# Kernel optimization log

Hardware: AMD Instinct MI355X
Metric: run time of the kernel (lower is better)

The kernel has to match this reference:

```python
import jax, jax.numpy as jnp
import numpy as np

NUM_HEADS = 16
LN_EPS = 1e-5


def setup_inputs() -> dict:
    key = jax.random.key(0)
    ks = jax.random.split(key, 6)
    b, s, d = 2, 2048, 1024
    scale = 1.0 / np.sqrt(d)
    return {
        "x": jax.random.normal(ks[0], (b, s, d), dtype=jnp.float32),
        "W_w": jax.random.normal(ks[1], (3 * d, d), dtype=jnp.float32) * scale,
        "W_b": jax.random.normal(ks[2], (3 * d,), dtype=jnp.float32) * 0.01,
        "proj_w": jax.random.normal(ks[3], (d, d), dtype=jnp.float32) * scale,
        "proj_b": jax.random.normal(ks[4], (d,), dtype=jnp.float32) * 0.01,
        "gamma": jnp.ones((d,), dtype=jnp.float32),
        "beta": jnp.zeros((d,), dtype=jnp.float32),
    }


def reference(x, W_w, W_b, proj_w, proj_b, gamma, beta):
    b, s, d = x.shape
    h = NUM_HEADS
    hd = d // h
    # fused QKV projection: [b,s,3d]
    qkv = x @ W_w.T + W_b
    q, k, v = jnp.split(qkv, 3, axis=-1)
    # [b,s,d] -> [b,h,s,hd]
    q, k, v = (z.reshape(b, s, h, hd).transpose(0, 2, 1, 3) for z in (q, k, v))
    # NOTE: original scales by sqrt(d), not sqrt(head_dim)
    attn = jnp.einsum('bhqd,bhkd->bhqk', q, k) / jnp.sqrt(jnp.asarray(d, x.dtype))
    attn_weights = jax.nn.softmax(attn, axis=-1)  # [b,h,s,s]
    o = jnp.einsum('bhqk,bhkd->bhqd', attn_weights, v)
    o = o.transpose(0, 2, 1, 3).reshape(b, s, d)
    out = o @ proj_w.T + proj_b  # dropout is identity at eval
    y = x + out
    mu = jnp.mean(y, axis=-1, keepdims=True)
    var = jnp.var(y, axis=-1, keepdims=True)
    y_norm = (y - mu) / jnp.sqrt(var + LN_EPS) * gamma + beta
    return (y_norm, attn_weights)
```

## Files before the change

### kernel.cpp

```cpp
#include <hip/hip_runtime.h>
#include <cstdint>

#define BB 2
#define SS 2048
#define DD 1024
#define HH 16
#define HDIM 64
#define MM (BB*SS)
#define N3 (3*DD)

typedef __attribute__((ext_vector_type(4))) float f32x4;
typedef __attribute__((ext_vector_type(8))) __bf16 bf16x8;

static __device__ __forceinline__ unsigned short f2bf_fast(float f) {
  __bf16 h = (__bf16)f;
  return __builtin_bit_cast(unsigned short, h);
}

static __device__ __forceinline__ uint4 pack8f(const float4 a, const float4 b) {
  union { unsigned short us[8]; uint4 v; } pk;
  pk.us[0] = f2bf_fast(a.x); pk.us[1] = f2bf_fast(a.y); pk.us[2] = f2bf_fast(a.z); pk.us[3] = f2bf_fast(a.w);
  pk.us[4] = f2bf_fast(b.x); pk.us[5] = f2bf_fast(b.y); pk.us[6] = f2bf_fast(b.z); pk.us[7] = f2bf_fast(b.w);
  return pk.v;
}

static __device__ __forceinline__ void gload16(const unsigned short* g, unsigned short* l) {
  __builtin_amdgcn_global_load_lds(
      (const __attribute__((address_space(1))) void*)g,
      (__attribute__((address_space(3))) void*)l, 16, 0, 0);
}

__global__ __launch_bounds__(256) void cvt_kernel(
    const float* __restrict__ x, const float* __restrict__ Ww,
    const float* __restrict__ pw,
    unsigned short* __restrict__ xb, unsigned short* __restrict__ Wwb,
    unsigned short* __restrict__ pwb) {
  const size_t i = ((size_t)blockIdx.x * 256 + threadIdx.x) * 8;
  const float* src;
  unsigned short* dst;
  if (i < 4194304u)       { src = x  + i;            dst = xb  + i; }
  else if (i < 7340032u)  { src = Ww + (i - 4194304u); dst = Wwb + (i - 4194304u); }
  else                    { src = pw + (i - 7340032u); dst = pwb + (i - 7340032u); }
  const float4* s4 = (const float4*)src;
  *(uint4*)dst = pack8f(s4[0], s4[1]);
}

__global__ __launch_bounds__(256) void gemm_qkv(
    const unsigned short* __restrict__ xb, const unsigned short* __restrict__ Wwb,
    const float* __restrict__ Wb,
    unsigned short* __restrict__ qb, unsigned short* __restrict__ kb,
    unsigned short* __restrict__ vbT) {
  __shared__ __align__(16) unsigned short As[128 * 32];
  __shared__ __align__(16) unsigned short Bs[128 * 32];
  const int t = threadIdx.x;
  const int l = t & 63, w = t >> 6;
  const int wr = w >> 1, wc = w & 1;
  const int m0 = blockIdx.y * 128, n0 = blockIdx.x * 128;
  f32x4 acc[4][4] = {};

  for (int kt = 0; kt < DD; kt += 32) {
    __syncthreads();
    #pragma unroll
    for (int i = 0; i < 2; ++i) {
      const int row = (i * 4 + w) * 16 + (l >> 2);
      const int cc = (l & 3) * 8;
      gload16(xb  + (size_t)(m0 + row) * DD + kt + cc, &As[(i * 4 + w) * 512]);
      gload16(Wwb + (size_t)(n0 + row) * DD + kt + cc, &Bs[(i * 4 + w) * 512]);
    }
    __syncthreads();
    bf16x8 a[4], b[4];
    #pragma unroll
    for (int i = 0; i < 4; ++i) {
      a[i] = __builtin_bit_cast(bf16x8, *(const uint4*)&As[(wr * 64 + i * 16 + (l & 15)) * 32 + (l >> 4) * 8]);
      b[i] = __builtin_bit_cast(bf16x8, *(const uint4*)&Bs[(wc * 64 + i * 16 + (l & 15)) * 32 + (l >> 4) * 8]);
    }
    #pragma unroll
    for (int i = 0; i < 4; ++i)
      #pragma unroll
      for (int j = 0; j < 4; ++j)
        acc[i][j] = __builtin_amdgcn_mfma_f32_16x16x32_bf16(a[i], b[j], acc[i][j], 0, 0, 0);
  }

  #pragma unroll
  for (int i = 0; i < 4; ++i)
    #pragma unroll
    for (int j = 0; j < 4; ++j)
      #pragma unroll
      for (int r = 0; r < 4; ++r) {
        const int row = m0 + wr * 64 + i * 16 + (l >> 4) * 4 + r;
        const int col = n0 + wc * 64 + j * 16 + (l & 15);
        const float v = acc[i][j][r] + Wb[col];
        const int bidx = row >> 11;
        const int srow = row & 2047;
        const int which = col >> 10;
        const int cc = col & 1023;
        const int head = cc >> 6;
        const int hd = cc & 63;
        if (which == 0) {
          qb[((size_t)((bidx * HH + head) * SS + srow)) * HDIM + hd] = f2bf_fast(v * 0.04508422f);
        } else if (which == 1) {
          kb[((size_t)((bidx * HH + head) * SS + srow)) * HDIM + hd] = f2bf_fast(v);
        } else {
          vbT[((size_t)(bidx * HH + head) * HDIM + hd) * SS + srow] = f2bf_fast(v);
        }
      }
}

__global__ __launch_bounds__(256) void attn_kernel(
    const unsigned short* __restrict__ qb,
    const unsigned short* __restrict__ kb,
    const unsigned short* __restrict__ vbT,
    unsigned short* __restrict__ ob,
    float* __restrict__ attn_out) {
  __shared__ __align__(16) unsigned short Ks[2][64 * 72];
  __shared__ __align__(16) unsigned short Vts[2][64 * 72];
  __shared__ __align__(16) unsigned short Ps[4 * 16 * 72];
  const int t = threadIdx.x;
  const int l = t & 63, w = t >> 6;
  const int bid = blockIdx.x;
  const int swz = (bid & 7) * 128 + (bid >> 3);
  const int bh = swz >> 5;
  const int q0 = (swz & 31) * 64;
  const size_t base = (size_t)bh * SS * HDIM;

  bf16x8 qa[2];
  #pragma unroll
  for (int kc = 0; kc < 2; ++kc)
    qa[kc] = __builtin_bit_cast(bf16x8,
        *(const uint4*)(qb + base + (size_t)(q0 + w * 16 + (l & 15)) * HDIM + kc * 32 + (l >> 4) * 8));

  const int srow = t >> 2;
  const int scol = (t & 3) * 16;
  const unsigned short* kg = kb + base + (size_t)srow * HDIM + scol;
  const unsigned short* vg = vbT + ((size_t)bh * HDIM + srow) * SS + scol;

  float lsum = 0.f;

  {
    const uint4* g = (const uint4*)kg;
    uint4 a0 = g[0], a1 = g[1];
    uint4* d = (uint4*)&Ks[0][srow * 72 + scol];
    d[0] = a0; d[1] = a1;
  }
  __syncthreads();
  for (int kt = 0; kt < SS; kt += 64) {
    const int cur = (kt >> 6) & 1;
    const bool more = (kt + 64) < SS;
    uint4 a0, a1;
    if (more) {
      const uint4* g = (const uint4*)(kg + (size_t)(kt + 64) * HDIM);
      a0 = g[0]; a1 = g[1];
    }
    f32x4 sf[4] = {};
    __builtin_amdgcn_s_setprio(1);
    #pragma unroll
    for (int kc = 0; kc < 2; ++kc)
      #pragma unroll
      for (int n = 0; n < 4; ++n) {
        bf16x8 kf = __builtin_bit_cast(bf16x8, *(const uint4*)&Ks[cur][(n * 16 + (l & 15)) * 72 + kc * 32 + (l >> 4) * 8]);
        sf[n] = __builtin_amdgcn_mfma_f32_16x16x32_bf16(kf, qa[kc], sf[n], 0, 0, 0);
      }
    __builtin_amdgcn_s_setprio(0);
    #pragma unroll
    for (int n = 0; n < 4; ++n)
      #pragma unroll
      for (int r = 0; r < 4; ++r)
        lsum += __builtin_amdgcn_exp2f(sf[n][r]);
    if (more) {
      uint4* d = (uint4*)&Ks[cur ^ 1][srow * 72 + scol];
      d[0] = a0; d[1] = a1;
    }
    __syncthreads();
  }

  lsum += __shfl_xor(lsum, 16);
  lsum += __shfl_xor(lsum, 32);
  const float rl = 1.0f / lsum;

  f32x4 of[4] = {};
  unsigned short* Pw = &Ps[w * 16 * 72];
  {
    const uint4* g = (const uint4*)kg;
    uint4 a0 = g[0], a1 = g[1];
    const uint4* gv = (const uint4*)vg;
    uint4 b0 = gv[0], b1 = gv[1];
    uint4* d = (uint4*)&Ks[0][srow * 72 + scol];  d[0] = a0; d[1] = a1;
    uint4* dv = (uint4*)&Vts[0][srow * 72 + scol]; dv[0] = b0; dv[1] = b1;
  }
  __syncthreads();
  float* prow = attn_out + ((size_t)bh * SS + (q0 + w * 16 + (l & 15))) * SS + (l >> 4) * 4;
  for (int kt = 0; kt < SS; kt += 64) {
    const int cur = (kt >> 6) & 1;
    const bool more = (kt + 64) < SS;
    uint4 a0, a1, b0, b1;
    if (more) {
      const uint4* g = (const uint4*)(kg + (size_t)(kt + 64) * HDIM);
      a0 = g[0]; a1 = g[1];
      const uint4* gv = (const uint4*)(vg + (kt + 64));
      b0 = gv[0]; b1 = gv[1];
    }
    f32x4 sf[4] = {};
    __builtin_amdgcn_s_setprio(1);
    #pragma unroll
    for (int kc = 0; kc < 2; ++kc)
      #pragma unroll
      for (int n = 0; n < 4; ++n) {
        bf16x8 kf = __builtin_bit_cast(bf16x8, *(const uint4*)&Ks[cur][(n * 16 + (l & 15)) * 72 + kc * 32 + (l >> 4) * 8]);
        sf[n] = __builtin_amdgcn_mfma_f32_16x16x32_bf16(kf, qa[kc], sf[n], 0, 0, 0);
      }
    __builtin_amdgcn_s_setprio(0);
    #pragma unroll
    for (int n = 0; n < 4; ++n) {
      float4 pv;
      pv.x = __builtin_amdgcn_exp2f(sf[n][0]) * rl;
      pv.y = __builtin_amdgcn_exp2f(sf[n][1]) * rl;
      pv.z = __builtin_amdgcn_exp2f(sf[n][2]) * rl;
      pv.w = __builtin_amdgcn_exp2f(sf[n][3]) * rl;
      __builtin_nontemporal_store(*(const f32x4*)&pv, (f32x4*)&prow[kt + n * 16]);
      ushort4 pb4;
      pb4.x = f2bf_fast(pv.x); pb4.y = f2bf_fast(pv.y);
      pb4.z = f2bf_fast(pv.z); pb4.w = f2bf_fast(pv.w);
      *(ushort4*)&Pw[(l & 15) * 72 + n * 16 + (l >> 4) * 4] = pb4;
    }
    #pragma unroll
    for (int kc = 0; kc < 2; ++kc) {
      bf16x8 pa = __builtin_bit_cast(bf16x8, *(const uint4*)&Pw[(l & 15) * 72 + kc * 32 + (l >> 4) * 8]);
      __builtin_amdgcn_s_setprio(1);
      #pragma unroll
      for (int n = 0; n < 4; ++n) {
        bf16x8 vf = __builtin_bit_cast(bf16x8, *(const uint4*)&Vts[cur][(n * 16 + (l & 15)) * 72 + kc * 32 + (l >> 4) * 8]);
        of[n] = __builtin_amdgcn_mfma_f32_16x16x32_bf16(pa, vf, of[n], 0, 0, 0);
      }
      __builtin_amdgcn_s_setprio(0);
    }
    if (more) {
      uint4* d = (uint4*)&Ks[cur ^ 1][srow * 72 + scol];  d[0] = a0; d[1] = a1;
      uint4* dv = (uint4*)&Vts[cur ^ 1][srow * 72 + scol]; dv[0] = b0; dv[1] = b1;
    }
    __syncthreads();
  }

  const int bidx = bh >> 4, h_ = bh & 15;
  #pragma unroll
  for (int n = 0; n < 4; ++n)
    #pragma unroll
    for (int r = 0; r < 4; ++r) {
      const int lr = (l >> 4) * 4 + r;
      const int srw = q0 + w * 16 + lr;
      const int col = h_ * 64 + n * 16 + (l & 15);
      ob[((size_t)bidx * SS + srw) * DD + col] = f2bf_fast(of[n][r]);
    }
}

__global__ __launch_bounds__(256) void gemm_proj(
    const unsigned short* __restrict__ ob, const unsigned short* __restrict__ pwb,
    const float* __restrict__ pb, const float* __restrict__ x,
    float* __restrict__ y) {
  __shared__ __align__(16) unsigned short As[128 * 32];
  __shared__ __align__(16) unsigned short Bs[128 * 32];
  const int t = threadIdx.x;
  const int l = t & 63, w = t >> 6;
  const int wr = w >> 1, wc = w & 1;
  const int m0 = blockIdx.y * 128, n0 = blockIdx.x * 128;
  f32x4 acc[4][4] = {};

  for (int kt = 0; kt < DD; kt += 32) {
    __syncthreads();
    #pragma unroll
    for (int i = 0; i < 2; ++i) {
      const int row = (i * 4 + w) * 16 + (l >> 2);
      const int cc = (l & 3) * 8;
      gload16(ob  + (size_t)(m0 + row) * DD + kt + cc, &As[(i * 4 + w) * 512]);
      gload16(pwb + (size_t)(n0 + row) * DD + kt + cc, &Bs[(i * 4 + w) * 512]);
    }
    __syncthreads();
    bf16x8 a[4], b[4];
    #pragma unroll
    for (int i = 0; i < 4; ++i) {
      a[i] = __builtin_bit_cast(bf16x8, *(const uint4*)&As[(wr * 64 + i * 16 + (l & 15)) * 32 + (l >> 4) * 8]);
      b[i] = __builtin_bit_cast(bf16x8, *(const uint4*)&Bs[(wc * 64 + i * 16 + (l & 15)) * 32 + (l >> 4) * 8]);
    }
    #pragma unroll
    for (int i = 0; i < 4; ++i)
      #pragma unroll
      for (int j = 0; j < 4; ++j)
        acc[i][j] = __builtin_amdgcn_mfma_f32_16x16x32_bf16(a[i], b[j], acc[i][j], 0, 0, 0);
  }
  #pragma unroll
  for (int i = 0; i < 4; ++i)
    #pragma unroll
    for (int j = 0; j < 4; ++j)
      #pragma unroll
      for (int r = 0; r < 4; ++r) {
        const int row = m0 + wr * 64 + i * 16 + (l >> 4) * 4 + r;
        const int col = n0 + wc * 64 + j * 16 + (l & 15);
        const size_t idx = (size_t)row * DD + col;
        y[idx] = acc[i][j][r] + pb[col] + x[idx];
      }
}

__global__ __launch_bounds__(256) void ln_kernel(
    float* __restrict__ y, const float* __restrict__ gamma,
    const float* __restrict__ beta) {
  const int row = blockIdx.x;
  const int t = threadIdx.x;
  const float4 v = ((const float4*)(y + (size_t)row * DD))[t];
  float s  = v.x + v.y + v.z + v.w;
  float s2 = v.x * v.x + v.y * v.y + v.z * v.z + v.w * v.w;
  #pragma unroll
  for (int off = 1; off < 64; off <<= 1) { s += __shfl_xor(s, off); s2 += __shfl_xor(s2, off); }
  __shared__ float red[8];
  const int l = t & 63, w = t >> 6;
  if (l == 0) { red[w] = s; red[4 + w] = s2; }
  __syncthreads();
  s  = red[0] + red[1] + red[2] + red[3];
  s2 = red[4] + red[5] + red[6] + red[7];
  const float mu = s * (1.0f / DD);
  const float var = s2 * (1.0f / DD) - mu * mu;
  const float rs = rsqrtf(var + 1e-5f);
  const float4 g  = ((const float4*)gamma)[t];
  const float4 be = ((const float4*)beta)[t];
  float4 o;
  o.x = (v.x - mu) * rs * g.x + be.x;
  o.y = (v.y - mu) * rs * g.y + be.y;
  o.z = (v.z - mu) * rs * g.z + be.z;
  o.w = (v.w - mu) * rs * g.w + be.w;
  ((float4*)(y + (size_t)row * DD))[t] = o;
}

extern "C" void kernel_launch(void* const* d_in, const int* in_sizes, int n_in,
                              void* d_out, int out_size, void* d_ws, size_t ws_size,
                              hipStream_t stream) {
  const float* x     = (const float*)d_in[0];
  const float* Ww    = (const float*)d_in[1];
  const float* Wb    = (const float*)d_in[2];
  const float* Pw    = (const float*)d_in[3];
  const float* Pb    = (const float*)d_in[4];
  const float* gamma = (const float*)d_in[5];
  const float* beta  = (const float*)d_in[6];

  float* out      = (float*)d_out;
  float* y_norm   = out;
  float* attn_out = out + (size_t)MM * DD;

  char* ws = (char*)d_ws;
  unsigned short* qb  = (unsigned short*)(ws);
  unsigned short* kb  = (unsigned short*)(ws +  8388608);
  unsigned short* vbT = (unsigned short*)(ws + 16777216);
  unsigned short* ob  = (unsigned short*)(ws + 25165824);
  unsigned short* xb  = (unsigned short*)(ws + 33554432);
  unsigned short* Wwb = (unsigned short*)(ws + 41943040);
  unsigned short* pwb = (unsigned short*)(ws + 48234496);

  cvt_kernel<<<4096, 256, 0, stream>>>(x, Ww, Pw, xb, Wwb, pwb);
  gemm_qkv<<<dim3(N3 / 128, MM / 128), 256, 0, stream>>>(xb, Wwb, Wb, qb, kb, vbT);
  attn_kernel<<<1024, 256, 0, stream>>>(qb, kb, vbT, ob, attn_out);
  gemm_proj<<<dim3(DD / 128, MM / 128), 256, 0, stream>>>(ob, pwb, Pb, x, y_norm);
  ln_kernel<<<MM, 256, 0, stream>>>(y_norm, gamma, beta);
}
```

Measured before the change: 266.1 us.

## Split attention key dimension across waves with register-resident K/V tiles

Restructures the attention kernel so that every wave computes all 64 query rows of the block, while each wave handles its own 16-key slice of every 64-key tile. K and V fragments are loaded straight from global memory into registers and prefetched one tile ahead, so the LDS staging buffers and the per-tile barriers go away. Row sums and output partials are combined across waves through LDS at the end. In exchange, the P·V MFMAs run half-empty because the K-operand is zero-padded from 16 to 32 values, register pressure goes up with 16 output accumulators, and the probability stores now cover 16-column slices per wave.

```diff
diff --git a/kernel.cpp b/kernel.cpp
--- a/kernel.cpp
+++ b/kernel.cpp
@@ -112,144 +112,163 @@
     const unsigned short* __restrict__ vbT,
     unsigned short* __restrict__ ob,
     float* __restrict__ attn_out) {
-  __shared__ __align__(16) unsigned short Ks[2][64 * 72];
-  __shared__ __align__(16) unsigned short Vts[2][64 * 72];
-  __shared__ __align__(16) unsigned short Ps[4 * 16 * 72];
+  __shared__ float Ored[4][64][68];
+  __shared__ float Lred[4][64];
   const int t = threadIdx.x;
   const int l = t & 63, w = t >> 6;
+  const int q_l = l & 15, hi = l >> 4;
   const int bid = blockIdx.x;
   const int swz = (bid & 7) * 128 + (bid >> 3);
   const int bh = swz >> 5;
   const int q0 = (swz & 31) * 64;
   const size_t base = (size_t)bh * SS * HDIM;
 
-  bf16x8 qa[2];
-  #pragma unroll
-  for (int kc = 0; kc < 2; ++kc)
-    qa[kc] = __builtin_bit_cast(bf16x8,
-        *(const uint4*)(qb + base + (size_t)(q0 + w * 16 + (l & 15)) * HDIM + kc * 32 + (l >> 4) * 8));
-
-  const int srow = t >> 2;
-  const int scol = (t & 3) * 16;
-  const unsigned short* kg = kb + base + (size_t)srow * HDIM + scol;
-  const unsigned short* vg = vbT + ((size_t)bh * HDIM + srow) * SS + scol;
-
-  float lsum = 0.f;
-
+  bf16x8 qa[4][2];
+  #pragma unroll
+  for (int j = 0; j < 4; ++j)
+    #pragma unroll
+    for (int kc = 0; kc < 2; ++kc)
+      qa[j][kc] = __builtin_bit_cast(bf16x8,
+          *(const uint4*)(qb + base + (size_t)(q0 + j * 16 + q_l) * HDIM + kc * 32 + hi * 8));
+
+  const unsigned short* kga = kb + base + (size_t)(w * 16 + q_l) * HDIM + hi * 8;
+  const unsigned short* vga = vbT + ((size_t)bh * HDIM + q_l) * SS + w * 16 + hi * 4;
+
+  float lsum[4] = {0.f, 0.f, 0.f, 0.f};
   {
-    const uint4* g = (const uint4*)kg;
-    uint4 a0 = g[0], a1 = g[1];
-    uint4* d = (uint4*)&Ks[0][srow * 72 + scol];
-    d[0] = a0; d[1] = a1;
+    uint4 k0 = *(const uint4*)(kga);
+    uint4 k1 = *(const uint4*)(kga + 32);
+    for (int kt = 0; kt < SS; kt += 64) {
+      const bool more = (kt + 64) < SS;
+      uint4 n0, n1;
+      if (more) {
+        n0 = *(const uint4*)(kga + (size_t)(kt + 64) * HDIM);
+        n1 = *(const uint4*)(kga + (size_t)(kt + 64) * HDIM + 32);
+      }
+      f32x4 sQ[4] = {};
+      const bf16x8 kf0 = __builtin_bit_cast(bf16x8, k0);
+      const bf16x8 kf1 = __builtin_bit_cast(bf16x8, k1);
+      __builtin_amdgcn_s_setprio(1);
+      #pragma unroll
+      for (int j = 0; j < 4; ++j) {
+        sQ[j] = __builtin_amdgcn_mfma_f32_16x16x32_bf16(kf0, qa[j][0], sQ[j], 0, 0, 0);
+        sQ[j] = __builtin_amdgcn_mfma_f32_16x16x32_bf16(kf1, qa[j][1], sQ[j], 0, 0, 0);
+      }
+      __builtin_amdgcn_s_setprio(0);
+      #pragma unroll
+      for (int j = 0; j < 4; ++j)
+        #pragma unroll
+        for (int r = 0; r < 4; ++r)
+          lsum[j] += __builtin_amdgcn_exp2f(sQ[j][r]);
+      k0 = n0; k1 = n1;
+    }
+  }
+  #pragma unroll
+  for (int j = 0; j < 4; ++j) {
+    float s = lsum[j];
+    s += __shfl_xor(s, 16);
+    s += __shfl_xor(s, 32);
+    lsum[j] = s;
+  }
+  if (hi == 0) {
+    #pragma unroll
+    for (int j = 0; j < 4; ++j) Lred[w][j * 16 + q_l] = lsum[j];
   }
   __syncthreads();
-  for (int kt = 0; kt < SS; kt += 64) {
-    const int cur = (kt >> 6) & 1;
-    const bool more = (kt + 64) < SS;
-    uint4 a0, a1;
-    if (more) {
-      const uint4* g = (const uint4*)(kg + (size_t)(kt + 64) * HDIM);
-      a0 = g[0]; a1 = g[1];
-    }
-    f32x4 sf[4] = {};
-    __builtin_amdgcn_s_setprio(1);
-    #pragma unroll
-    for (int kc = 0; kc < 2; ++kc)
-      #pragma unroll
-      for (int n = 0; n < 4; ++n) {
-        bf16x8 kf = __builtin_bit_cast(bf16x8, *(const uint4*)&Ks[cur][(n * 16 + (l & 15)) * 72 + kc * 32 + (l >> 4) * 8]);
-        sf[n] = __builtin_amdgcn_mfma_f32_16x16x32_bf16(kf, qa[kc], sf[n], 0, 0, 0);
-      }
-    __builtin_amdgcn_s_setprio(0);
-    #pragma unroll
-    for (int n = 0; n < 4; ++n)
-      #pragma unroll
-      for (int r = 0; r < 4; ++r)
-        lsum += __builtin_amdgcn_exp2f(sf[n][r]);
-    if (more) {
-      uint4* d = (uint4*)&Ks[cur ^ 1][srow * 72 + scol];
-      d[0] = a0; d[1] = a1;
-    }
-    __syncthreads();
-  }
-
-  lsum += __shfl_xor(lsum, 16);
-  lsum += __shfl_xor(lsum, 32);
-  const float rl = 1.0f / lsum;
-
-  f32x4 of[4] = {};
-  unsigned short* Pw = &Ps[w * 16 * 72];
+  float rl[4];
+  #pragma unroll
+  for (int j = 0; j < 4; ++j)
+    rl[j] = 1.0f / (Lred[0][j * 16 + q_l] + Lred[1][j * 16 + q_l] +
+                    Lred[2][j * 16 + q_l] + Lred[3][j * 16 + q_l]);
+
+  float* pbs[4];
+  #pragma unroll
+  for (int j = 0; j < 4; ++j)
+    pbs[j] = attn_out + ((size_t)bh * SS + (q0 + j * 16 + q_l)) * SS + w * 16 + hi * 4;
+
+  f32x4 of[4][4] = {};
   {
-    const uint4* g = (const uint4*)kg;
-    uint4 a0 = g[0], a1 = g[1];
-    const uint4* gv = (const uint4*)vg;
-    uint4 b0 = gv[0], b1 = gv[1];
-    uint4* d = (uint4*)&Ks[0][srow * 72 + scol];  d[0] = a0; d[1] = a1;
-    uint4* dv = (uint4*)&Vts[0][srow * 72 + scol]; dv[0] = b0; dv[1] = b1;
-  }
+    uint4 k0 = *(const uint4*)(kga);
+    uint4 k1 = *(const uint4*)(kga + 32);
+    uint2 vv[4];
+    #pragma unroll
+    for (int d4 = 0; d4 < 4; ++d4)
+      vv[d4] = *(const uint2*)(vga + (size_t)(d4 * 16) * SS);
+    for (int kt = 0; kt < SS; kt += 64) {
+      const bool more = (kt + 64) < SS;
+      uint4 n0, n1; uint2 nv[4];
+      if (more) {
+        n0 = *(const uint4*)(kga + (size_t)(kt + 64) * HDIM);
+        n1 = *(const uint4*)(kga + (size_t)(kt + 64) * HDIM + 32);
+        #pragma unroll
+        for (int d4 = 0; d4 < 4; ++d4)
+          nv[d4] = *(const uint2*)(vga + (size_t)(d4 * 16) * SS + kt + 64);
+      }
+      f32x4 sQ[4] = {};
+      const bf16x8 kf0 = __builtin_bit_cast(bf16x8, k0);
+      const bf16x8 kf1 = __builtin_bit_cast(bf16x8, k1);
+      __builtin_amdgcn_s_setprio(1);
+      #pragma unroll
+      for (int j = 0; j < 4; ++j) {
+        sQ[j] = __builtin_amdgcn_mfma_f32_16x16x32_bf16(kf0, qa[j][0], sQ[j], 0, 0, 0);
+        sQ[j] = __builtin_amdgcn_mfma_f32_16x16x32_bf16(kf1, qa[j][1], sQ[j], 0, 0, 0);
+      }
+      __builtin_amdgcn_s_setprio(0);
+      bf16x8 pbp[4];
+      #pragma unroll
+      for (int j = 0; j < 4; ++j) {
+        float4 pv;
+        pv.x = __builtin_amdgcn_exp2f(sQ[j][0]) * rl[j];
+        pv.y = __builtin_amdgcn_exp2f(sQ[j][1]) * rl[j];
+        pv.z = __builtin_amdgcn_exp2f(sQ[j][2]) * rl[j];
+        pv.w = __builtin_amdgcn_exp2f(sQ[j][3]) * rl[j];
+        __builtin_nontemporal_store(*(const f32x4*)&pv, (f32x4*)(pbs[j] + kt));
+        union { unsigned short us[8]; uint4 v; } pk;
+        pk.us[0] = f2bf_fast(pv.x); pk.us[1] = f2bf_fast(pv.y);
+        pk.us[2] = f2bf_fast(pv.z); pk.us[3] = f2bf_fast(pv.w);
+        pk.us[4] = 0; pk.us[5] = 0; pk.us[6] = 0; pk.us[7] = 0;
+        pbp[j] = __builtin_bit_cast(bf16x8, pk.v);
+      }
+      __builtin_amdgcn_s_setprio(1);
+      #pragma unroll
+      for (int d4 = 0; d4 < 4; ++d4) {
+        uint4 vp; vp.x = vv[d4].x; vp.y = vv[d4].y; vp.z = 0u; vp.w = 0u;
+        const bf16x8 vfp = __builtin_bit_cast(bf16x8, vp);
+        #pragma unroll
+        for (int j = 0; j < 4; ++j)
+          of[d4][j] = __builtin_amdgcn_mfma_f32_16x16x32_bf16(vfp, pbp[j], of[d4][j], 0, 0, 0);
+      }
+      __builtin_amdgcn_s_setprio(0);
+      k0 = n0; k1 = n1;
+      #pragma unroll
+      for (int d4 = 0; d4 < 4; ++d4) vv[d4] = nv[d4];
+    }
+  }
+
+  #pragma unroll
+  for (int d4 = 0; d4 < 4; ++d4)
+    #pragma unroll
+    for (int j = 0; j < 4; ++j)
+      *(f32x4*)&Ored[w][j * 16 + q_l][d4 * 16 + hi * 4] = of[d4][j];
   __syncthreads();
-  float* prow = attn_out + ((size_t)bh * SS + (q0 + w * 16 + (l & 15))) * SS + (l >> 4) * 4;
-  for (int kt = 0; kt < SS; kt += 64) {
-    const int cur = (kt >> 6) & 1;
-    const bool more = (kt + 64) < SS;
-    uint4 a0, a1, b0, b1;
-    if (more) {
-      const uint4* g = (const uint4*)(kg + (size_t)(kt + 64) * HDIM);
-      a0 = g[0]; a1 = g[1];
-      const uint4* gv = (const uint4*)(vg + (kt + 64));
-      b0 = gv[0]; b1 = gv[1];
-    }
-    f32x4 sf[4] = {};
-    __builtin_amdgcn_s_setprio(1);
-    #pragma unroll
-    for (int kc = 0; kc < 2; ++kc)
-      #pragma unroll
-      for (int n = 0; n < 4; ++n) {
-        bf16x8 kf = __builtin_bit_cast(bf16x8, *(const uint4*)&Ks[cur][(n * 16 + (l & 15)) * 72 + kc * 32 + (l >> 4) * 8]);
-        sf[n] = __builtin_amdgcn_mfma_f32_16x16x32_bf16(kf, qa[kc], sf[n], 0, 0, 0);
-      }
-    __builtin_amdgcn_s_setprio(0);
-    #pragma unroll
-    for (int n = 0; n < 4; ++n) {
-      float4 pv;
-      pv.x = __builtin_amdgcn_exp2f(sf[n][0]) * rl;
-      pv.y = __builtin_amdgcn_exp2f(sf[n][1]) * rl;
-      pv.z = __builtin_amdgcn_exp2f(sf[n][2]) * rl;
-      pv.w = __builtin_amdgcn_exp2f(sf[n][3]) * rl;
-      __builtin_nontemporal_store(*(const f32x4*)&pv, (f32x4*)&prow[kt + n * 16]);
-      ushort4 pb4;
-      pb4.x = f2bf_fast(pv.x); pb4.y = f2bf_fast(pv.y);
-      pb4.z = f2bf_fast(pv.z); pb4.w = f2bf_fast(pv.w);
-      *(ushort4*)&Pw[(l & 15) * 72 + n * 16 + (l >> 4) * 4] = pb4;
-    }
-    #pragma unroll
-    for (int kc = 0; kc < 2; ++kc) {
-      bf16x8 pa = __builtin_bit_cast(bf16x8, *(const uint4*)&Pw[(l & 15) * 72 + kc * 32 + (l >> 4) * 8]);
-      __builtin_amdgcn_s_setprio(1);
-      #pragma unroll
-      for (int n = 0; n < 4; ++n) {
-        bf16x8 vf = __builtin_bit_cast(bf16x8, *(const uint4*)&Vts[cur][(n * 16 + (l & 15)) * 72 + kc * 32 + (l >> 4) * 8]);
-        of[n] = __builtin_amdgcn_mfma_f32_16x16x32_bf16(pa, vf, of[n], 0, 0, 0);
-      }
-      __builtin_amdgcn_s_setprio(0);
-    }
-    if (more) {
-      uint4* d = (uint4*)&Ks[cur ^ 1][srow * 72 + scol];  d[0] = a0; d[1] = a1;
-      uint4* dv = (uint4*)&Vts[cur ^ 1][srow * 72 + scol]; dv[0] = b0; dv[1] = b1;
-    }
-    __syncthreads();
-  }
-
   const int bidx = bh >> 4, h_ = bh & 15;
-  #pragma unroll
-  for (int n = 0; n < 4; ++n)
-    #pragma unroll
-    for (int r = 0; r < 4; ++r) {
-      const int lr = (l >> 4) * 4 + r;
-      const int srw = q0 + w * 16 + lr;
-      const int col = h_ * 64 + n * 16 + (l & 15);
-      ob[((size_t)bidx * SS + srw) * DD + col] = f2bf_fast(of[n][r]);
-    }
+  const int qf = w * 16 + q_l;
+  union { unsigned short us[16]; uint4 v[2]; } opk;
+  #pragma unroll
+  for (int c4 = 0; c4 < 4; ++c4) {
+    const int d0 = hi * 16 + c4 * 4;
+    f32x4 s = *(const f32x4*)&Ored[0][qf][d0];
+    s += *(const f32x4*)&Ored[1][qf][d0];
+    s += *(const f32x4*)&Ored[2][qf][d0];
+    s += *(const f32x4*)&Ored[3][qf][d0];
+    opk.us[c4 * 4 + 0] = f2bf_fast(s[0]);
+    opk.us[c4 * 4 + 1] = f2bf_fast(s[1]);
+    opk.us[c4 * 4 + 2] = f2bf_fast(s[2]);
+    opk.us[c4 * 4 + 3] = f2bf_fast(s[3]);
+  }
+  unsigned short* orow = ob + ((size_t)bidx * SS + (q0 + qf)) * DD + h_ * 64 + hi * 16;
+  *(uint4*)orow = opk.v[0];
+  *(uint4*)(orow + 8) = opk.v[1];
 }
 
 __global__ __launch_bounds__(256) void gemm_proj(
```

Result: no change. 262.6 us (-1.3%).
